# Kernel optimization log

Hardware: AMD Instinct MI355X
Metric: run time of the kernel (lower is better)

## Reference

```python
import jax, jax.numpy as jnp
import numpy as np

N_E = 1024
E_DIM = 256
TAU = 0.5
BETA = 0.25
LAMB = 0.1
EPS = 1e-10


def setup_inputs() -> dict:
    key = jax.random.key(0)
    k1, k2, k3 = jax.random.split(key, 3)
    z = jax.random.normal(k1, (16, 1024, E_DIM), dtype=jnp.float32)
    # kaiming-normal-initialized codebook (std = sqrt(2 / fan_in))
    emb = jax.random.normal(k2, (N_E, E_DIM), dtype=jnp.float32) * np.sqrt(2.0 / E_DIM)
    u = jax.random.uniform(k3, (16 * 1024, N_E), dtype=jnp.float32)
    return {"z": z, "emb": emb, "u": u}


def reference(z, emb, u):
    zf = z.reshape(-1, E_DIM)                                  # [N, e_dim]
    # squared euclidean distances to each code: ||z||^2 + ||e||^2 - 2 z.e
    d = (jnp.sum(zf * zf, axis=1, keepdims=True)
         + jnp.sum(emb * emb, axis=1)
         - 2.0 * jnp.matmul(zf, emb.T))                        # [N, n_e]
    # gumbel-softmax (hard, straight-through) on logits = -d
    g = -jnp.log(-jnp.log(u + EPS) + EPS)
    y_soft = jax.nn.softmax((-d + g) / TAU, axis=-1)
    idx = jnp.argmax(y_soft, axis=-1)
    y_hard = jax.nn.one_hot(idx, N_E, dtype=y_soft.dtype)
    probs = y_hard + y_soft - jax.lax.stop_gradient(y_soft)    # [N, n_e]
    z_q = jnp.matmul(probs, emb).reshape(z.shape)
    # orthogonality loss on the codebook gram matrix
    gram = jnp.matmul(emb, emb.T)
    ortho = jnp.mean((gram - jnp.eye(N_E, dtype=emb.dtype)) ** 2) / (N_E ** 2)
    emb_loss = jnp.mean((jax.lax.stop_gradient(z_q) - z) ** 2)
    commit = BETA * jnp.mean((z_q - jax.lax.stop_gradient(z)) ** 2)
    loss = emb_loss + BETA * commit + LAMB * ortho
    z_q_st = z + jax.lax.stop_gradient(z_q - z)
    e_mean = jnp.mean(probs, axis=0)
    perplexity = jnp.exp(-jnp.sum(e_mean * jnp.log(e_mean + EPS)))
    return loss, z_q_st, perplexity
```

## Files before the change

### kernel.cpp

```cpp
#include <hip/hip_runtime.h>
#include <math.h>
#include <stdint.h>


#define NROWS 16384
#define NE    1024
#define ED    256
#define EPSF  1e-10f
#define INV2048 4.8828125e-4f
#define BM 64
#define BN 64
#define SCW 68

typedef _Float16 half_t;
typedef __attribute__((ext_vector_type(4))) _Float16 half4;
typedef __attribute__((ext_vector_type(8))) _Float16 half8;
typedef __attribute__((ext_vector_type(16))) float floatx16;
typedef unsigned long long u64;

__device__ __forceinline__ void gl_lds16(const void* g, void* l) {
    __builtin_amdgcn_global_load_lds(
        (const __attribute__((address_space(1))) uint32_t*)g,
        (__attribute__((address_space(3))) uint32_t*)l, 16, 0, 0);
}

__device__ __forceinline__ u64 packMax(float v, int code) {
    unsigned int b   = __float_as_uint(v);
    unsigned int key = (b & 0x80000000u) ? ~b : (b | 0x80000000u);
    return ((u64)key << 32) | (unsigned int)(NE - 1 - code);
}

__global__ __launch_bounds__(256) void vq_prep(
        const float* __restrict__ z, const float* __restrict__ emb,
        half_t* __restrict__ zh, half_t* __restrict__ zl,
        half_t* __restrict__ eh, half_t* __restrict__ el,
        float* __restrict__ enorm, float* __restrict__ znorm,
        u64* __restrict__ best)
{
    const int gid = blockIdx.x * 256 + threadIdx.x;
    const int ZQ8 = NROWS * ED / 8;
    if (gid < ZQ8) {
        const float4 v0 = ((const float4*)z)[(size_t)gid * 2];
        const float4 v1 = ((const float4*)z)[(size_t)gid * 2 + 1];
        const float x[8] = {v0.x, v0.y, v0.z, v0.w, v1.x, v1.y, v1.z, v1.w};
        half8 h, l;
        float s = 0.f;
#pragma unroll
        for (int i = 0; i < 8; ++i) {
            const half_t hi = (half_t)x[i];
            h[i] = hi; l[i] = (half_t)((x[i] - (float)hi) * 2048.0f);
            s = fmaf(x[i], x[i], s);
        }
        *(half8*)&zh[(size_t)gid * 8] = h;
        *(half8*)&zl[(size_t)gid * 8] = l;
#pragma unroll
        for (int o = 16; o; o >>= 1) s += __shfl_down(s, o, 32);
        if ((threadIdx.x & 31) == 0) znorm[gid >> 5] = s;
    } else {
        const int eg = gid - ZQ8;
        const float4 v0 = ((const float4*)emb)[(size_t)eg * 2];
        const float4 v1 = ((const float4*)emb)[(size_t)eg * 2 + 1];
        const float x[8] = {v0.x, v0.y, v0.z, v0.w, v1.x, v1.y, v1.z, v1.w};
        half8 h, l;
        float s = 0.f;
#pragma unroll
        for (int i = 0; i < 8; ++i) {
            const half_t hi = (half_t)x[i];
            h[i] = hi; l[i] = (half_t)((x[i] - (float)hi) * 2048.0f);
            s = fmaf(x[i], x[i], s);
        }
        *(half8*)&eh[(size_t)eg * 8] = h;
        *(half8*)&el[(size_t)eg * 8] = l;
#pragma unroll
        for (int o = 16; o; o >>= 1) s += __shfl_down(s, o, 32);
        if ((threadIdx.x & 31) == 0) enorm[eg >> 5] = s;
        if (eg < NROWS) best[eg] = 0ull;
    }
}

__global__ __launch_bounds__(256, 4) void vq_gemm(
        const half_t* __restrict__ zh, const half_t* __restrict__ zl,
        const half_t* __restrict__ eh, const half_t* __restrict__ el,
        const float* __restrict__ u, const float* __restrict__ enorm,
        u64* __restrict__ best)
{
    __shared__ __align__(16) char smem[32768];
    half_t* Ah = (half_t*)smem;
    half_t* Al = (half_t*)(smem + 8192);
    half_t* Bh = (half_t*)(smem + 16384);
    half_t* Bl = (half_t*)(smem + 24576);
    float (*Sc)[SCW] = (float(*)[SCW])smem;
    u64* parr = (u64*)(smem + 17408);

    const int t    = threadIdx.x;
    const int w    = t >> 6;
    const int lane = t & 63;
    const int lrow = lane & 31;
    const int hw   = lane >> 5;

    const int bid = blockIdx.x;
    const int xcd = bid & 7, c = bid >> 3;
    const int m0 = (xcd * 32 + (c >> 4)) * BM;
    const int n0 = (c & 15) * BN;
    const int wm = (w >> 1) * 32, wn = (w & 1) * 32;

    size_t gaoff[2], gboff[2];
#pragma unroll
    for (int it = 0; it < 2; ++it) {
        const int s = it * 256 + t;
        const int row = s >> 3;
        const int cc = (s & 7) ^ (row & 7);
        gaoff[it] = (size_t)(m0 + row) * ED + cc * 8;
        gboff[it] = (size_t)(n0 + row) * ED + cc * 8;
    }

    auto STAGE = [&](int kc) {
#pragma unroll
        for (int it = 0; it < 2; ++it) {
            const int ldso = (it * 256 + w * 64) * 8;
            gl_lds16(zh + gaoff[it] + kc, Ah + ldso);
            gl_lds16(zl + gaoff[it] + kc, Al + ldso);
            gl_lds16(eh + gboff[it] + kc, Bh + ldso);
            gl_lds16(el + gboff[it] + kc, Bl + ldso);
        }
    };

    floatx16 accH = {};
    floatx16 accX = {};

    STAGE(0);
    for (int kc = 0; kc < ED; kc += 64) {
        __syncthreads();
#pragma unroll
        for (int ks = 0; ks < 4; ++ks) {
            const int cch = ks * 2 + hw;
            const int ar = wm + lrow;
            const int br = wn + lrow;
            const int sa = ar * 8 + (cch ^ (ar & 7));
            const int sb = br * 8 + (cch ^ (br & 7));
            const half8 ah = *(const half8*)&Ah[sa * 8];
            const half8 al = *(const half8*)&Al[sa * 8];
            const half8 bh = *(const half8*)&Bh[sb * 8];
            const half8 bl = *(const half8*)&Bl[sb * 8];
            accH = __builtin_amdgcn_mfma_f32_32x32x16_f16(ah, bh, accH, 0, 0, 0);
            accX = __builtin_amdgcn_mfma_f32_32x32x16_f16(ah, bl, accX, 0, 0, 0);
            accX = __builtin_amdgcn_mfma_f32_32x32x16_f16(al, bh, accX, 0, 0, 0);
        }
        __syncthreads();
        if (kc + 64 < ED) STAGE(kc + 64);
    }

    const int   col0 = n0 + wn + lrow;
    const float en0  = enorm[col0];
#pragma unroll
    for (int r = 0; r < 16; ++r) {
        const int lr = wm + (r & 3) + ((r >> 2) << 3) + (hw << 2);
        const float d  = accH[r] + accX[r] * INV2048;
        const float uv = u[(size_t)(m0 + lr) * NE + col0];
        const float g  = -__logf(-__logf(uv + EPSF) + EPSF);
        Sc[lr][wn + lrow] = 2.f * d - en0 + g;
    }
    __syncthreads();

    {
        const int row = t >> 2;
        const int ch  = (t & 3) << 4;
        float bv = -1e38f; int bc = 0;
#pragma unroll
        for (int q = 0; q < 4; ++q) {
            const float4 v = *(const float4*)&Sc[row][ch + (q << 2)];
            const int cc = n0 + ch + (q << 2);
            if (v.x > bv) { bv = v.x; bc = cc; }
            if (v.y > bv) { bv = v.y; bc = cc + 1; }
            if (v.z > bv) { bv = v.z; bc = cc + 2; }
            if (v.w > bv) { bv = v.w; bc = cc + 3; }
        }
        parr[t] = packMax(bv, bc);
    }
    __syncthreads();
    if (t < 64) {
        const u64 a = parr[(t << 2)],     b = parr[(t << 2) + 1];
        const u64 e = parr[(t << 2) + 2], f = parr[(t << 2) + 3];
        const u64 m1 = a > b ? a : b;
        const u64 m2 = e > f ? e : f;
        atomicMax(&best[m0 + t], m1 > m2 ? m1 : m2);
    }
}

__global__ __launch_bounds__(256) void vq_outstore(
        const float* __restrict__ emb, const u64* __restrict__ best,
        const float* __restrict__ znorm, const float* __restrict__ u,
        int* __restrict__ idxArr, double* __restrict__ partial,
        float* __restrict__ out)
{
    __shared__ int   ridx[8];
    __shared__ float rmse[8];
    const int t  = threadIdx.x;
    const int m0 = blockIdx.x * 8;

    if (t < 8) {
        const u64 p = best[m0 + t];
        const unsigned int key = (unsigned int)(p >> 32);
        const int code = NE - 1 - (int)(p & 0xFFFFFFFFu);
        ridx[t] = code;
        idxArr[m0 + t] = code;
        const unsigned int b = (key & 0x80000000u) ? (key ^ 0x80000000u) : ~key;
        const float s  = __uint_as_float(b);
        const float uv = u[(size_t)(m0 + t) * NE + code];
        const float g  = -__logf(-__logf(uv + EPSF) + EPSF);
        rmse[t] = znorm[m0 + t] - s + g;
    }
    __syncthreads();
    if (t == 0) {
        double acc = 0.0;
#pragma unroll
        for (int r = 0; r < 8; ++r) acc += (double)rmse[r];
        partial[blockIdx.x] = acc;
    }

#pragma unroll
    for (int rr = 0; rr < 8; ++rr) {
        const int j = ridx[rr];
        out[1 + (size_t)(m0 + rr) * ED + t] = emb[(size_t)j * ED + t];
    }
}

__global__ __launch_bounds__(256) void vq_fin(
        const int* __restrict__ idxArr, const double* __restrict__ partial,
        float* __restrict__ out)
{
    __shared__ int    hist[NE];
    __shared__ double redl[4], redp[4];
    const int t = threadIdx.x;

    for (int i = t; i < NE; i += 256) hist[i] = 0;
    __syncthreads();

    for (int r = t; r < NROWS; r += 256)
        atomicAdd(&hist[idxArr[r]], 1);

    double lsum = 0.0;
    for (int b = t; b < NROWS / 8; b += 256)
        lsum += partial[b];
    __syncthreads();

    double psum = 0.0;
    for (int i = t; i < NE; i += 256) {
        const float em = (float)hist[i] / (float)NROWS;
        psum += (double)(em * logf(em + EPSF));
    }

#pragma unroll
    for (int o = 32; o; o >>= 1) { lsum += __shfl_down(lsum, o); psum += __shfl_down(psum, o); }
    if ((t & 63) == 0) { redl[t >> 6] = lsum; redp[t >> 6] = psum; }
    __syncthreads();
    if (t == 0) {
        const double mse = (redl[0] + redl[1] + redl[2] + redl[3])
                           / (double)((size_t)NROWS * ED);
        const double tot = redp[0] + redp[1] + redp[2] + redp[3];
        out[0] = (float)(mse * 1.0625);
        out[1 + (size_t)NROWS * ED] = (float)exp(-tot);
    }
}

extern "C" void kernel_launch(void* const* d_in, const int* in_sizes, int n_in,
                              void* d_out, int out_size, void* d_ws, size_t ws_size,
                              hipStream_t stream) {
    const float* z   = (const float*)d_in[0];
    const float* emb = (const float*)d_in[1];
    const float* u   = (const float*)d_in[2];
    float* out = (float*)d_out;

    float*  enorm    = (float*)((char*)d_ws + 5120);
    u64*    best     = (u64*)((char*)d_ws + 9216);
    float*  znorm    = (float*)((char*)d_ws + 140288);
    int*    idxArr   = (int*)((char*)d_ws + 205824);
    double* partial  = (double*)((char*)d_ws + 271360);
    const size_t small_end = 287744;

    const size_t zsplit = (size_t)NROWS * ED * 2;
    const size_t esplit = (size_t)NE * ED * 2;
    const bool bigws = ws_size >= small_end + 2 * zsplit + 2 * esplit;

    half_t *zh, *zl, *eh, *el;
    if (bigws) {
        char* big = (char*)d_ws + small_end;
        zh = (half_t*)big;
        zl = (half_t*)(big + zsplit);
        eh = (half_t*)(big + 2 * zsplit);
        el = (half_t*)(big + 2 * zsplit + esplit);
    } else {
        zh = (half_t*)((char*)d_out + 8);
        zl = (half_t*)((char*)d_out + 8 + zsplit);
        eh = (half_t*)((char*)d_ws + small_end);
        el = (half_t*)((char*)d_ws + small_end + esplit);
    }

    vq_prep<<<(NROWS * ED / 8 + NE * ED / 8) / 256, 256, 0, stream>>>(
        z, emb, zh, zl, eh, el, enorm, znorm, best);
    vq_gemm<<<(NROWS / BM) * (NE / BN), 256, 0, stream>>>(
        zh, zl, eh, el, u, enorm, best);
    vq_outstore<<<NROWS / 8, 256, 0, stream>>>(
        emb, best, znorm, u, idxArr, partial, out);
    vq_fin<<<1, 256, 0, stream>>>(idxArr, partial, out);
}
```

Baseline: 174.3 us.

## Transpose MFMA operands so each lane holds one z-row, reduce argmax in registers

Swaps the MFMA operand roles so the accumulator is laid out with codebook entries along rows and z rows along lanes. This lets each lane compute the per-row argmax directly in registers, then combine with one cross-half shuffle, instead of spilling scores to an LDS scratch tile and rescanning it. The uniform-noise loads are issued as contiguous float4 loads before the GEMM loop and pinned with an empty asm, so their latency overlaps the matrix work. The change removes one barrier and the LDS score traffic, at the cost of holding extra registers live across the main loop.

```diff
diff --git a/kernel.cpp b/kernel.cpp
--- a/kernel.cpp
+++ b/kernel.cpp
@@ -10,7 +10,6 @@
 #define INV2048 4.8828125e-4f
 #define BM 64
 #define BN 64
-#define SCW 68
 
 typedef _Float16 half_t;
 typedef __attribute__((ext_vector_type(4))) _Float16 half4;
@@ -85,12 +84,11 @@
         u64* __restrict__ best)
 {
     __shared__ __align__(16) char smem[32768];
-    half_t* Ah = (half_t*)smem;
-    half_t* Al = (half_t*)(smem + 8192);
-    half_t* Bh = (half_t*)(smem + 16384);
-    half_t* Bl = (half_t*)(smem + 24576);
-    float (*Sc)[SCW] = (float(*)[SCW])smem;
-    u64* parr = (u64*)(smem + 17408);
+    half_t* Ch = (half_t*)smem;
+    half_t* Cl = (half_t*)(smem + 8192);
+    half_t* Zh = (half_t*)(smem + 16384);
+    half_t* Zl = (half_t*)(smem + 24576);
+    u64* parr = (u64*)smem;
 
     const int t    = threadIdx.x;
     const int w    = t >> 6;
@@ -102,28 +100,39 @@
     const int xcd = bid & 7, c = bid >> 3;
     const int m0 = (xcd * 32 + (c >> 4)) * BM;
     const int n0 = (c & 15) * BN;
-    const int wm = (w >> 1) * 32, wn = (w & 1) * 32;
-
-    size_t gaoff[2], gboff[2];
+    const int wr = w >> 1, wc = w & 1;
+
+    size_t gcoff[2], gzoff[2];
 #pragma unroll
     for (int it = 0; it < 2; ++it) {
         const int s = it * 256 + t;
         const int row = s >> 3;
         const int cc = (s & 7) ^ (row & 7);
-        gaoff[it] = (size_t)(m0 + row) * ED + cc * 8;
-        gboff[it] = (size_t)(n0 + row) * ED + cc * 8;
+        gcoff[it] = (size_t)(n0 + row) * ED + cc * 8;
+        gzoff[it] = (size_t)(m0 + row) * ED + cc * 8;
     }
 
     auto STAGE = [&](int kc) {
 #pragma unroll
         for (int it = 0; it < 2; ++it) {
             const int ldso = (it * 256 + w * 64) * 8;
-            gl_lds16(zh + gaoff[it] + kc, Ah + ldso);
-            gl_lds16(zl + gaoff[it] + kc, Al + ldso);
-            gl_lds16(eh + gboff[it] + kc, Bh + ldso);
-            gl_lds16(el + gboff[it] + kc, Bl + ldso);
+            gl_lds16(eh + gcoff[it] + kc, Ch + ldso);
+            gl_lds16(el + gcoff[it] + kc, Cl + ldso);
+            gl_lds16(zh + gzoff[it] + kc, Zh + ldso);
+            gl_lds16(zl + gzoff[it] + kc, Zl + ldso);
         }
     };
+
+    const int myrow = m0 + wr * 32 + lrow;
+    const int cbase = n0 + wc * 32 + (hw << 2);
+    float4 uf[4];
+    {
+        const float* up = u + (size_t)myrow * NE + cbase;
+        uf[0] = *(const float4*)(up);
+        uf[1] = *(const float4*)(up + 8);
+        uf[2] = *(const float4*)(up + 16);
+        uf[3] = *(const float4*)(up + 24);
+    }
 
     floatx16 accH = {};
     floatx16 accX = {};
@@ -134,56 +143,63 @@
 #pragma unroll
         for (int ks = 0; ks < 4; ++ks) {
             const int cch = ks * 2 + hw;
-            const int ar = wm + lrow;
-            const int br = wn + lrow;
-            const int sa = ar * 8 + (cch ^ (ar & 7));
-            const int sb = br * 8 + (cch ^ (br & 7));
-            const half8 ah = *(const half8*)&Ah[sa * 8];
-            const half8 al = *(const half8*)&Al[sa * 8];
-            const half8 bh = *(const half8*)&Bh[sb * 8];
-            const half8 bl = *(const half8*)&Bl[sb * 8];
-            accH = __builtin_amdgcn_mfma_f32_32x32x16_f16(ah, bh, accH, 0, 0, 0);
-            accX = __builtin_amdgcn_mfma_f32_32x32x16_f16(ah, bl, accX, 0, 0, 0);
-            accX = __builtin_amdgcn_mfma_f32_32x32x16_f16(al, bh, accX, 0, 0, 0);
+            const int cr = wc * 32 + lrow;
+            const int zr = wr * 32 + lrow;
+            const int sc_ = cr * 8 + (cch ^ (cr & 7));
+            const int sz_ = zr * 8 + (cch ^ (zr & 7));
+            const half8 ch8 = *(const half8*)&Ch[sc_ * 8];
+            const half8 cl8 = *(const half8*)&Cl[sc_ * 8];
+            const half8 zh8 = *(const half8*)&Zh[sz_ * 8];
+            const half8 zl8 = *(const half8*)&Zl[sz_ * 8];
+            accH = __builtin_amdgcn_mfma_f32_32x32x16_f16(ch8, zh8, accH, 0, 0, 0);
+            accX = __builtin_amdgcn_mfma_f32_32x32x16_f16(ch8, zl8, accX, 0, 0, 0);
+            accX = __builtin_amdgcn_mfma_f32_32x32x16_f16(cl8, zh8, accX, 0, 0, 0);
+        }
+        if (kc == 0) {
+#pragma unroll
+            for (int q = 0; q < 4; ++q)
+                asm volatile("" :: "v"(uf[q].x), "v"(uf[q].y),
+                                   "v"(uf[q].z), "v"(uf[q].w));
         }
         __syncthreads();
         if (kc + 64 < ED) STAGE(kc + 64);
     }
 
-    const int   col0 = n0 + wn + lrow;
-    const float en0  = enorm[col0];
+    float4 ef[4];
+    {
+        const float* ep = enorm + cbase;
+        ef[0] = *(const float4*)(ep);
+        ef[1] = *(const float4*)(ep + 8);
+        ef[2] = *(const float4*)(ep + 16);
+        ef[3] = *(const float4*)(ep + 24);
+    }
+    u64 bestp = 0ull;
 #pragma unroll
     for (int r = 0; r < 16; ++r) {
-        const int lr = wm + (r & 3) + ((r >> 2) << 3) + (hw << 2);
+        const int q = r >> 2, j = r & 3;
+        const float uv = ((const float*)&uf[q])[j];
+        const float en = ((const float*)&ef[q])[j];
         const float d  = accH[r] + accX[r] * INV2048;
-        const float uv = u[(size_t)(m0 + lr) * NE + col0];
         const float g  = -__logf(-__logf(uv + EPSF) + EPSF);
-        Sc[lr][wn + lrow] = 2.f * d - en0 + g;
-    }
-    __syncthreads();
-
+        const float sc = 2.f * d - en + g;
+        const u64 pm = packMax(sc, cbase + j + (q << 3));
+        if (pm > bestp) bestp = pm;
+    }
     {
-        const int row = t >> 2;
-        const int ch  = (t & 3) << 4;
-        float bv = -1e38f; int bc = 0;
-#pragma unroll
-        for (int q = 0; q < 4; ++q) {
-            const float4 v = *(const float4*)&Sc[row][ch + (q << 2)];
-            const int cc = n0 + ch + (q << 2);
-            if (v.x > bv) { bv = v.x; bc = cc; }
-            if (v.y > bv) { bv = v.y; bc = cc + 1; }
-            if (v.z > bv) { bv = v.z; bc = cc + 2; }
-            if (v.w > bv) { bv = v.w; bc = cc + 3; }
-        }
-        parr[t] = packMax(bv, bc);
+        const unsigned int lo = (unsigned int)bestp;
+        const unsigned int hi = (unsigned int)(bestp >> 32);
+        const unsigned int lo2 = __shfl_down(lo, 32);
+        const unsigned int hi2 = __shfl_down(hi, 32);
+        const u64 o = ((u64)hi2 << 32) | lo2;
+        if (o > bestp) bestp = o;
+    }
+    if (lrow == lane) {
+        parr[(wr * 32 + lrow) * 2 + wc] = bestp;
     }
     __syncthreads();
     if (t < 64) {
-        const u64 a = parr[(t << 2)],     b = parr[(t << 2) + 1];
-        const u64 e = parr[(t << 2) + 2], f = parr[(t << 2) + 3];
-        const u64 m1 = a > b ? a : b;
-        const u64 m2 = e > f ? e : f;
-        atomicMax(&best[m0 + t], m1 > m2 ? m1 : m2);
+        const u64 a = parr[t * 2], b = parr[t * 2 + 1];
+        atomicMax(&best[m0 + t], a > b ? a : b);
     }
 }
 
```

New measurement: 176.0 us. About the same (+1.0%).
